# Performance work log

Measured on AMD Instinct MI355X. Metric: run time of the kernel, lower is better.

Reference implementation:

```python
import jax, jax.numpy as jnp
import numpy as np

ALPHA = 20.0


def setup_inputs() -> dict:
    key = jax.random.key(0)
    k1, k2 = jax.random.split(key)
    N, C = 8192, 8
    output = jax.random.normal(k1, (N, C), dtype=jnp.float32)
    target = jax.random.randint(k2, (N,), 0, C, dtype=jnp.int64)
    return {"output": output, "target": target}


def reference(output, target):
    # output: [N, C] logits, target: [N] int labels in [0, C-1]
    probs = jax.nn.softmax(output, axis=1)
    dtype = probs.dtype
    C = output.shape[1]
    total_auc = jnp.zeros((), dtype)
    valid_count = jnp.zeros((), dtype)
    for class_idx in range(C):  # fixed small class loop, matches original
        p = probs[:, class_idx]                      # [N]
        pos = (target == class_idx).astype(dtype)    # [N]
        neg = 1.0 - pos                              # [N]
        n_pos = pos.sum()
        n_neg = neg.sum()
        # pairwise sigmoid(alpha * (p_i - p_j)) masked to (pos_i, neg_j) pairs
        s = jax.nn.sigmoid(ALPHA * (p[:, None] - p[None, :]))  # [N, N]
        pair_sum = jnp.einsum('i,ij,j->', pos, s, neg)
        valid = jnp.logical_and(n_pos > 0, n_neg > 0)
        mean_auc_c = jnp.where(valid, pair_sum / jnp.maximum(n_pos * n_neg, 1.0), 0.0)
        total_auc = total_auc + mean_auc_c
        valid_count = valid_count + valid.astype(dtype)
    loss = jnp.where(valid_count > 0, 1.0 - total_auc / jnp.maximum(valid_count, 1.0), 0.0)
    return loss
```

## Files before the change

kernel.cpp:

```cpp
#include <hip/hip_runtime.h>

#define SCALE 28.853900817779268f
#define L2E   1.4426950408889634f
#define M 2048
#define T 1024
#define CPC 32
#define QB (M/CPC)

__device__ __forceinline__ float fexp2(float x){ return __builtin_amdgcn_exp2f(x); }
__device__ __forceinline__ float frcp (float x){ return __builtin_amdgcn_rcpf(x); }
__device__ __forceinline__ float Gfun(int x, float invM){
  return frcp(1.0f + fexp2(SCALE * (float)(x - (M-1)) * invM));
}

#define WRED64(x) { _Pragma("unroll") for (int _o = 32; _o; _o >>= 1) x += __shfl_down(x, _o, 64); }
#define ALOAD(p) __hip_atomic_load((p), __ATOMIC_RELAXED, __HIP_MEMORY_SCOPE_AGENT)

__global__ __launch_bounds__(1024)
void k_fused(const float* __restrict__ logits, const int* __restrict__ tgt,
             float* __restrict__ out, unsigned* __restrict__ ticket,
             float* __restrict__ gpart, int* __restrict__ ccnt, int N){
  const int b = blockIdx.x, NB = (int)gridDim.x;
  const int c = b >> 5, ch = b & (CPC-1);
  const int tid = threadIdx.x, lane = tid & 63, w = tid >> 6;
  const float invM = 1.0f / (float)M;
  const int s = ch & 1;

  __shared__ int    HP[M];
  __shared__ float2 G2[M];
  __shared__ int    Pkc[64];
  __shared__ int    wnp[16];
  __shared__ float  rw[16];
  __shared__ float  scs[8];
  __shared__ int    lastflag;

  ((int2*)HP)[tid] = make_int2(0, 0);
  G2[tid]        = make_float2(Gfun(2*tid + s,          invM),
                               Gfun(2*tid + s + 1,      invM));
  G2[tid + 1024] = make_float2(Gfun(2*(tid+1024) + s,   invM),
                               Gfun(2*(tid+1024) + s+1, invM));
  __syncthreads();

  const float4* l4 = (const float4*)logits;
  #pragma unroll 2
  for (int i = tid; i < N; i += T){
    float4 A = l4[2*i], B4 = l4[2*i+1];
    float e0=fexp2(A.x *L2E), e1=fexp2(A.y *L2E), e2=fexp2(A.z *L2E), e3=fexp2(A.w *L2E);
    float e4=fexp2(B4.x*L2E), e5=fexp2(B4.y*L2E), e6=fexp2(B4.z*L2E), e7=fexp2(B4.w*L2E);
    float sm = ((e0+e1)+(e2+e3))+((e4+e5)+(e6+e7));
    float ec = e0;
    ec=(c==1)?e1:ec; ec=(c==2)?e2:ec; ec=(c==3)?e3:ec;
    ec=(c==4)?e4:ec; ec=(c==5)?e5:ec; ec=(c==6)?e6:ec; ec=(c==7)?e7:ec;
    float p = ec * frcp(sm);
    int bin = min((int)(p * (float)M), M-1);
    int inc = 1 + ((tgt[i] == c) ? (1 << 16) : 0);
    atomicAdd(&HP[bin], inc);
  }
  __syncthreads();

  float Hj0, Hj1; int np_part;
  {
    int2 hp = ((const int2*)HP)[tid];
    int p0 = hp.x >> 16, p1 = hp.y >> 16;
    np_part = p0 + p1;
    Hj0 = (float)((hp.x & 0xFFFF) - p0);
    Hj1 = (float)((hp.y & 0xFFFF) - p1);
  }
  if (tid < 64) Pkc[tid] = HP[ch + CPC*tid];
  WRED64(np_part)
  if (lane == 0) wnp[w] = np_part;
  __syncthreads();

  const int jb = ((2046 + ch - s) >> 1) - tid;
  const int pkv = Pkc[lane];
  float t0 = 0.f, t1 = 0.f, t2 = 0.f, t3 = 0.f;
  #pragma unroll
  for (int q = 0; q < QB; q += 4){
    #pragma unroll
    for (int u = 0; u < 4; ++u){
      int pq = __builtin_amdgcn_readlane(pkv, q + u);
      float Pk = (float)(pq >> 16);
      float2 gg = G2[jb + 16*(q + u)];
      float term = fmaf(Hj0, gg.y, Hj1 * gg.x);
      if (u == 0) t0 = fmaf(Pk, term, t0);
      if (u == 1) t1 = fmaf(Pk, term, t1);
      if (u == 2) t2 = fmaf(Pk, term, t2);
      if (u == 3) t3 = fmaf(Pk, term, t3);
    }
  }
  float tot = (t0 + t1) + (t2 + t3);
  WRED64(tot)
  if (lane == 0) rw[w] = tot;
  __syncthreads();
  if (tid == 0){
    float bt = 0.f;
    #pragma unroll
    for (int i = 0; i < 16; ++i) bt += rw[i];
    atomicExch(&gpart[b], bt);
    if (ch == 0){
      int snp = 0;
      #pragma unroll
      for (int i = 0; i < 16; ++i) snp += wnp[i];
      atomicExch(&ccnt[c], snp);
    }
    __threadfence();
    unsigned old = atomicAdd(ticket, 1u);
    lastflag = ((old % (unsigned)NB) == (unsigned)(NB - 1));
  }
  __syncthreads();
  if (!lastflag) return;

  if (tid == 0) __threadfence();
  __syncthreads();
  if (tid < 256){
    int c2 = tid >> 5, l = tid & 31;
    float sp = ALOAD(&gpart[c2*CPC + l]);
    #pragma unroll
    for (int o = 16; o; o >>= 1) sp += __shfl_down(sp, o, 32);
    if (l == 0) scs[c2] = sp;
  }
  __syncthreads();
  if (tid < 8){
    int np = ALOAD(&ccnt[tid]);
    int nn = N - np;
    bool valid = (np > 0 && nn > 0);
    float t = valid ? scs[tid] / ((float)np * (float)nn) : 0.f;
    float f = valid ? 1.f : 0.f;
    #pragma unroll
    for (int o = 4; o; o >>= 1){
      t += __shfl_down(t, o, 8);
      f += __shfl_down(f, o, 8);
    }
    if (tid == 0) out[0] = (f > 0.f) ? (1.0f - t / f) : 0.0f;
  }
}

extern "C" void kernel_launch(void* const* d_in, const int* in_sizes, int n_in,
                              void* d_out, int out_size, void* d_ws, size_t ws_size,
                              hipStream_t stream) {
    const float* logits = (const float*)d_in[0];
    const int*   tgt    = (const int*)d_in[1];
    float* out = (float*)d_out;
    int N = in_sizes[1];

    unsigned* ticket = (unsigned*)d_ws;
    float* gpart = (float*)d_ws + 32;
    int*   ccnt  = (int*)((float*)d_ws + 288);

    k_fused<<<8*CPC, T, 0, stream>>>(logits, tgt, out, ticket, gpart, ccnt, N);
}
```

Measured before the change: 17.11 us.

## Use per-class completion tickets and batch logits loads for fixed N

```diff
diff --git a/kernel.cpp b/kernel.cpp
--- a/kernel.cpp
+++ b/kernel.cpp
@@ -15,12 +15,14 @@
 
 #define WRED64(x) { _Pragma("unroll") for (int _o = 32; _o; _o >>= 1) x += __shfl_down(x, _o, 64); }
 #define ALOAD(p) __hip_atomic_load((p), __ATOMIC_RELAXED, __HIP_MEMORY_SCOPE_AGENT)
+#define AADD(p,v) __hip_atomic_fetch_add((p),(v), __ATOMIC_RELAXED, __HIP_MEMORY_SCOPE_AGENT)
 
 __global__ __launch_bounds__(1024)
 void k_fused(const float* __restrict__ logits, const int* __restrict__ tgt,
-             float* __restrict__ out, unsigned* __restrict__ ticket,
-             float* __restrict__ gpart, int* __restrict__ ccnt, int N){
-  const int b = blockIdx.x, NB = (int)gridDim.x;
+             float* __restrict__ out, unsigned* __restrict__ gtick,
+             unsigned* __restrict__ ctick, float* __restrict__ csum,
+             int* __restrict__ vld, float* __restrict__ gpart, int N){
+  const int b = blockIdx.x;
   const int c = b >> 5, ch = b & (CPC-1);
   const int tid = threadIdx.x, lane = tid & 63, w = tid >> 6;
   const float invM = 1.0f / (float)M;
@@ -31,8 +33,7 @@
   __shared__ int    Pkc[64];
   __shared__ int    wnp[16];
   __shared__ float  rw[16];
-  __shared__ float  scs[8];
-  __shared__ int    lastflag;
+  __shared__ int    cflagS, gflagS;
 
   ((int2*)HP)[tid] = make_int2(0, 0);
   G2[tid]        = make_float2(Gfun(2*tid + s,          invM),
@@ -42,19 +43,43 @@
   __syncthreads();
 
   const float4* l4 = (const float4*)logits;
-  #pragma unroll 2
-  for (int i = tid; i < N; i += T){
-    float4 A = l4[2*i], B4 = l4[2*i+1];
-    float e0=fexp2(A.x *L2E), e1=fexp2(A.y *L2E), e2=fexp2(A.z *L2E), e3=fexp2(A.w *L2E);
-    float e4=fexp2(B4.x*L2E), e5=fexp2(B4.y*L2E), e6=fexp2(B4.z*L2E), e7=fexp2(B4.w*L2E);
-    float sm = ((e0+e1)+(e2+e3))+((e4+e5)+(e6+e7));
-    float ec = e0;
-    ec=(c==1)?e1:ec; ec=(c==2)?e2:ec; ec=(c==3)?e3:ec;
-    ec=(c==4)?e4:ec; ec=(c==5)?e5:ec; ec=(c==6)?e6:ec; ec=(c==7)?e7:ec;
-    float p = ec * frcp(sm);
-    int bin = min((int)(p * (float)M), M-1);
-    int inc = 1 + ((tgt[i] == c) ? (1 << 16) : 0);
-    atomicAdd(&HP[bin], inc);
+  if (N == (T<<3)){
+    #pragma unroll
+    for (int h = 0; h < 2; ++h){
+      float4 Ar[4], Br[4]; int tv[4];
+      #pragma unroll
+      for (int r = 0; r < 4; ++r){
+        int i = tid + (((h<<2)|r) << 10);
+        Ar[r] = l4[2*i]; Br[r] = l4[2*i+1]; tv[r] = tgt[i];
+      }
+      #pragma unroll
+      for (int r = 0; r < 4; ++r){
+        float e0=fexp2(Ar[r].x*L2E), e1=fexp2(Ar[r].y*L2E),
+              e2=fexp2(Ar[r].z*L2E), e3=fexp2(Ar[r].w*L2E);
+        float e4=fexp2(Br[r].x*L2E), e5=fexp2(Br[r].y*L2E),
+              e6=fexp2(Br[r].z*L2E), e7=fexp2(Br[r].w*L2E);
+        float sm = ((e0+e1)+(e2+e3))+((e4+e5)+(e6+e7));
+        float ec = e0;
+        ec=(c==1)?e1:ec; ec=(c==2)?e2:ec; ec=(c==3)?e3:ec;
+        ec=(c==4)?e4:ec; ec=(c==5)?e5:ec; ec=(c==6)?e6:ec; ec=(c==7)?e7:ec;
+        float p = ec * frcp(sm);
+        int bin = min((int)(p * (float)M), M-1);
+        atomicAdd(&HP[bin], 1 + ((tv[r] == c) ? (1 << 16) : 0));
+      }
+    }
+  } else {
+    for (int i = tid; i < N; i += T){
+      float4 A = l4[2*i], B4 = l4[2*i+1];
+      float e0=fexp2(A.x *L2E), e1=fexp2(A.y *L2E), e2=fexp2(A.z *L2E), e3=fexp2(A.w *L2E);
+      float e4=fexp2(B4.x*L2E), e5=fexp2(B4.y*L2E), e6=fexp2(B4.z*L2E), e7=fexp2(B4.w*L2E);
+      float sm = ((e0+e1)+(e2+e3))+((e4+e5)+(e6+e7));
+      float ec = e0;
+      ec=(c==1)?e1:ec; ec=(c==2)?e2:ec; ec=(c==3)?e3:ec;
+      ec=(c==4)?e4:ec; ec=(c==5)?e5:ec; ec=(c==6)?e6:ec; ec=(c==7)?e7:ec;
+      float p = ec * frcp(sm);
+      int bin = min((int)(p * (float)M), M-1);
+      atomicAdd(&HP[bin], 1 + ((tgt[i] == c) ? (1 << 16) : 0));
+    }
   }
   __syncthreads();
 
@@ -92,40 +117,48 @@
   WRED64(tot)
   if (lane == 0) rw[w] = tot;
   __syncthreads();
+
   if (tid == 0){
     float bt = 0.f;
     #pragma unroll
     for (int i = 0; i < 16; ++i) bt += rw[i];
     atomicExch(&gpart[b], bt);
-    if (ch == 0){
+    __threadfence();
+    unsigned oc = AADD(&ctick[c*16], 1u);
+    cflagS = ((oc & (CPC-1)) == (CPC-1));
+  }
+  __syncthreads();
+  if (cflagS){
+    if (tid == 0) __threadfence();
+    __syncthreads();
+    float sred = 0.f;
+    if (tid < CPC){
+      sred = ALOAD(&gpart[c*CPC + tid]);
+      #pragma unroll
+      for (int o = 16; o; o >>= 1) sred += __shfl_down(sred, o, 32);
+    }
+    if (tid == 0){
       int snp = 0;
       #pragma unroll
       for (int i = 0; i < 16; ++i) snp += wnp[i];
-      atomicExch(&ccnt[c], snp);
+      int nn = N - snp;
+      bool v = (snp > 0 && nn > 0);
+      float tc = v ? sred / ((float)snp * (float)nn) : 0.f;
+      atomicExch(&csum[c], tc);
+      atomicExch(&vld[c],  v ? 1 : 0);
+      __threadfence();
+      unsigned og = AADD(gtick, 1u);
+      gflagS = ((og & 7u) == 7u);
     }
-    __threadfence();
-    unsigned old = atomicAdd(ticket, 1u);
-    lastflag = ((old % (unsigned)NB) == (unsigned)(NB - 1));
-  }
+  } else if (tid == 0) gflagS = 0;
   __syncthreads();
-  if (!lastflag) return;
+  if (!gflagS) return;
 
   if (tid == 0) __threadfence();
   __syncthreads();
-  if (tid < 256){
-    int c2 = tid >> 5, l = tid & 31;
-    float sp = ALOAD(&gpart[c2*CPC + l]);
-    #pragma unroll
-    for (int o = 16; o; o >>= 1) sp += __shfl_down(sp, o, 32);
-    if (l == 0) scs[c2] = sp;
-  }
-  __syncthreads();
   if (tid < 8){
-    int np = ALOAD(&ccnt[tid]);
-    int nn = N - np;
-    bool valid = (np > 0 && nn > 0);
-    float t = valid ? scs[tid] / ((float)np * (float)nn) : 0.f;
-    float f = valid ? 1.f : 0.f;
+    float t = ALOAD(&csum[tid]);
+    float f = (float)ALOAD(&vld[tid]);
     #pragma unroll
     for (int o = 4; o; o >>= 1){
       t += __shfl_down(t, o, 8);
@@ -143,9 +176,13 @@
     float* out = (float*)d_out;
     int N = in_sizes[1];
 
-    unsigned* ticket = (unsigned*)d_ws;
-    float* gpart = (float*)d_ws + 32;
-    int*   ccnt  = (int*)((float*)d_ws + 288);
+    unsigned* ws    = (unsigned*)d_ws;
+    unsigned* gtick = ws;
+    unsigned* ctick = ws + 16;
+    float*    csum  = (float*)(ws + 160);
+    int*      vld   = (int*)  (ws + 168);
+    float*    gpart = (float*)(ws + 192);
 
-    k_fused<<<8*CPC, T, 0, stream>>>(logits, tgt, out, ticket, gpart, ccnt, N);
+    k_fused<<<8*CPC, T, 0, stream>>>(logits, tgt, out, gtick, ctick,
+                                     csum, vld, gpart, N);
 }
```

Result: slower. 17.78 us (+3.9%).
